# Kernel optimization log

Hardware: AMD Instinct MI355X
Metric: run time of the kernel (lower is better)

Reference implementation:

```python
import jax, jax.numpy as jnp
import numpy as np

D_MODEL = 1024
N_HEADS = 16
D_HEAD = D_MODEL // N_HEADS


def setup_inputs() -> dict:
    key = jax.random.key(0)
    ks = jax.random.split(key, 9)
    B, S = 2, 2048
    s = 0.02
    return {
        "x": jax.random.normal(ks[0], (B, S, D_MODEL), dtype=jnp.float32),
        "Wq": jax.random.normal(ks[1], (D_MODEL, D_MODEL), dtype=jnp.float32) * s,
        "bq": jnp.zeros((D_MODEL,), dtype=jnp.float32),
        "Wk": jax.random.normal(ks[2], (D_MODEL, D_MODEL), dtype=jnp.float32) * s,
        "bk": jnp.zeros((D_MODEL,), dtype=jnp.float32),
        "Wv": jax.random.normal(ks[3], (D_MODEL, D_MODEL), dtype=jnp.float32) * s,
        "bv": jnp.zeros((D_MODEL,), dtype=jnp.float32),
        "Wo": jax.random.normal(ks[4], (D_MODEL, D_MODEL), dtype=jnp.float32) * s,
        "bo": jnp.zeros((D_MODEL,), dtype=jnp.float32),
    }


def reference(x, Wq, bq, Wk, bk, Wv, bv, Wo, bo):
    B, S, _ = x.shape
    # projections -> [B, H, S, Dh]
    def split_heads(t):
        return t.reshape(B, S, N_HEADS, D_HEAD).transpose(0, 2, 1, 3)
    Q = split_heads(x @ Wq + bq)
    K = split_heads(x @ Wk + bk)
    V = split_heads(x @ Wv + bv)
    scores = jnp.einsum('bhqd,bhkd->bhqk', Q, K)  # [B,H,S,S]
    mask = jnp.tril(jnp.ones((S, S), dtype=bool))
    # NB: original masks BEFORE scaling (mask fill -1e9 then /sqrt(d_head))
    scores = jnp.where(mask[None, None], scores, jnp.float32(-1e9))
    scores = scores / jnp.sqrt(jnp.float32(D_HEAD))
    attn = jax.nn.softmax(scores, axis=-1)
    ctx = jnp.einsum('bhqk,bhkd->bhqd', attn, V)
    ctx = ctx.transpose(0, 2, 1, 3).reshape(B, S, D_MODEL)
    return ctx @ Wo + bo
```

## Files before the change

kernel.cpp:

```cpp
#include <hip/hip_runtime.h>

typedef __bf16 bf16;
typedef __bf16 bf16x8 __attribute__((ext_vector_type(8)));
typedef __bf16 bf16x4 __attribute__((ext_vector_type(4)));
typedef float  f32x4  __attribute__((ext_vector_type(4)));

#define D_MODEL 1024
#define S_LEN   2048
#define NHEAD   16
#define DHEAD   64
#define BATCH   2
#define MROWS   (BATCH * S_LEN)

#define QSCALE 0.18033688011112042f

__device__ __forceinline__ void gld_lds16(const void* g, void* lds_base) {
    __builtin_amdgcn_global_load_lds(
        (const __attribute__((address_space(1))) void*)g,
        (__attribute__((address_space(3))) void*)lds_base, 16, 0, 0);
}

__global__ void prep_kernel(const float* __restrict__ x,
                            const float* __restrict__ W0, const float* __restrict__ W1,
                            const float* __restrict__ W2, const float* __restrict__ W3,
                            bf16* __restrict__ xb, bf16* __restrict__ Wt) {
    int tx = threadIdx.x, ty = threadIdx.y;
    if (blockIdx.z == 4) {
        int tid = ty * 32 + tx;
        size_t base = ((size_t)blockIdx.y * 32 + blockIdx.x) * 4096;
#pragma unroll
        for (int j = 0; j < 4; j++) {
            size_t i = base + (size_t)(j * 256 + tid) * 4;
            f32x4 v = *(const f32x4*)(x + i);
            bf16x4 o;
            o[0] = (bf16)v[0]; o[1] = (bf16)v[1]; o[2] = (bf16)v[2]; o[3] = (bf16)v[3];
            *(bf16x4*)(xb + i) = o;
        }
        return;
    }
    __shared__ float tile[32][33];
    const float* W = (blockIdx.z == 0) ? W0 : (blockIdx.z == 1) ? W1
                   : (blockIdx.z == 2) ? W2 : W3;
    int n0 = blockIdx.x * 32, k0 = blockIdx.y * 32;
#pragma unroll
    for (int j = 0; j < 4; j++)
        tile[ty + 8 * j][tx] = W[(size_t)(k0 + ty + 8 * j) * D_MODEL + n0 + tx];
    __syncthreads();
    bf16* out = Wt + (size_t)blockIdx.z * D_MODEL * D_MODEL;
#pragma unroll
    for (int j = 0; j < 4; j++)
        out[(size_t)(n0 + ty + 8 * j) * D_MODEL + k0 + tx] = (bf16)tile[tx][ty + 8 * j];
}

template <int MODE>
__global__ __launch_bounds__(256, 2) void gemm_kernel(
    const bf16* __restrict__ A, const bf16* __restrict__ Bt,
    const float* __restrict__ b0, const float* __restrict__ b1, const float* __restrict__ b2,
    bf16* __restrict__ Qo, bf16* __restrict__ Ko, bf16* __restrict__ Vto,
    float* __restrict__ Co) {
    __shared__ bf16 sA[128 * 32];
    __shared__ bf16 sB[128 * 32];
    const int t = threadIdx.x;
    const int wave = t >> 6, lane = t & 63;
    const int wm = wave >> 1, wn = wave & 1;
    const int quad = lane >> 4, m16 = lane & 15;
    const int row0 = blockIdx.y * 128, col0 = blockIdx.x * 128;
    const int K = D_MODEL;

    f32x4 acc[4][4];
#pragma unroll
    for (int i = 0; i < 4; i++)
#pragma unroll
        for (int j = 0; j < 4; j++) acc[i][j] = (f32x4){0.f, 0.f, 0.f, 0.f};

    for (int kk = 0; kk < K; kk += 32) {
#pragma unroll
        for (int i = 0; i < 2; i++) {
            int cb = i * 256 + wave * 64;
            int c  = cb + lane;
            int r  = c >> 2, kg = c & 3;
            gld_lds16(A  + (size_t)(row0 + r) * K + kk + kg * 8, (char*)sA + cb * 16);
            gld_lds16(Bt + (size_t)(col0 + r) * K + kk + kg * 8, (char*)sB + cb * 16);
        }
        __syncthreads();
        bf16x8 af[4], bfr[4];
#pragma unroll
        for (int mi = 0; mi < 4; mi++)
            af[mi] = *(const bf16x8*)&sA[(wm * 64 + mi * 16 + m16) * 32 + quad * 8];
#pragma unroll
        for (int ni = 0; ni < 4; ni++)
            bfr[ni] = *(const bf16x8*)&sB[(wn * 64 + ni * 16 + m16) * 32 + quad * 8];
#pragma unroll
        for (int mi = 0; mi < 4; mi++)
#pragma unroll
            for (int ni = 0; ni < 4; ni++)
                acc[mi][ni] = __builtin_amdgcn_mfma_f32_16x16x32_bf16(
                    af[mi], bfr[ni], acc[mi][ni], 0, 0, 0);
        __syncthreads();
    }

    if (MODE == 1) {
#pragma unroll
        for (int mi = 0; mi < 4; mi++) {
            int r0 = row0 + wm * 64 + mi * 16 + quad * 4;
#pragma unroll
            for (int ni = 0; ni < 4; ni++) {
                int col = col0 + wn * 64 + ni * 16 + m16;
                float bias = b0[col];
#pragma unroll
                for (int r = 0; r < 4; r++)
                    Co[(size_t)(r0 + r) * D_MODEL + col] = acc[mi][ni][r] + bias;
            }
        }
    } else {
        int sel = col0 >> 10;
        const float* bias_arr = (sel == 0) ? b0 : (sel == 1) ? b1 : b2;
#pragma unroll
        for (int mi = 0; mi < 4; mi++) {
            int s0g = row0 + wm * 64 + mi * 16 + quad * 4;
            int b = s0g >> 11, ss0 = s0g & 2047;
#pragma unroll
            for (int ni = 0; ni < 4; ni++) {
                int col = col0 + wn * 64 + ni * 16 + m16;
                int cn = col & 1023;
                int h = cn >> 6, d = cn & 63;
                float bias = bias_arr[cn];
                if (sel < 2) {
                    bf16* dst = (sel == 0) ? Qo : Ko;
                    float scl = (sel == 0) ? QSCALE : 1.0f;
                    size_t base = (((size_t)b * NHEAD + h) * S_LEN);
#pragma unroll
                    for (int r = 0; r < 4; r++)
                        dst[(base + ss0 + r) * DHEAD + d] = (bf16)((acc[mi][ni][r] + bias) * scl);
                } else {
                    bf16x4 pk;
#pragma unroll
                    for (int r = 0; r < 4; r++) pk[r] = (bf16)(acc[mi][ni][r] + bias);
                    *(bf16x4*)(Vto + (((size_t)b * NHEAD + h) * DHEAD + d) * S_LEN + ss0) = pk;
                }
            }
        }
    }
}

__global__ __launch_bounds__(256, 2) void attn_kernel(
    const bf16* __restrict__ Q, const bf16* __restrict__ K,
    const bf16* __restrict__ Vt, bf16* __restrict__ ctx) {
    __shared__ bf16 Kt_s[3][64 * 64];
    __shared__ bf16 Vt_s[3][64 * 64];
    __shared__ bf16 P_s[4][2][16 * 72];

    const int t = threadIdx.x, wave = t >> 6, lane = t & 63;
    const int quad = lane >> 4, m16 = lane & 15;
    const int bh = blockIdx.y, p = blockIdx.x;
    const int tT[2] = {p, 31 - p};
    const int nt = 32 - p;
    const size_t base = (size_t)bh * S_LEN * DHEAD;

    bf16x8 aq[2][2];
#pragma unroll
    for (int it = 0; it < 2; it++)
#pragma unroll
        for (int kst = 0; kst < 2; kst++)
            aq[it][kst] = *(const bf16x8*)(Q + base
                + (size_t)(tT[it] * 64 + wave * 16 + m16) * DHEAD + kst * 32 + quad * 8);

    f32x4 o[2][4];
#pragma unroll
    for (int it = 0; it < 2; it++)
#pragma unroll
        for (int di = 0; di < 4; di++) o[it][di] = (f32x4){0.f, 0.f, 0.f, 0.f};
    float l_acc[2] = {0.f, 0.f};

    auto stage = [&](int j, int buf) {
#pragma unroll
        for (int i = 0; i < 2; i++) {
            int cb = i * 256 + wave * 64;
            int c  = cb + lane;
            int pos = c >> 3, g = c & 7;
            int gk = g ^ (pos & 7);
            gld_lds16(K  + base + (size_t)(j * 64 + pos) * DHEAD + gk * 8,
                      (char*)&Kt_s[buf][0] + cb * 16);
            gld_lds16(Vt + base + (size_t)pos * S_LEN + j * 64 + gk * 8,
                      (char*)&Vt_s[buf][0] + cb * 16);
        }
    };

    stage(0, 0);
    if (nt > 1) stage(1, 1);

    for (int j = 0; j < nt; ++j) {
        if (j + 1 < nt) asm volatile("s_waitcnt vmcnt(4)\n\ts_barrier" ::: "memory");
        else            asm volatile("s_waitcnt vmcnt(0)\n\ts_barrier" ::: "memory");
        if (j + 2 < nt) stage(j + 2, (j + 2) % 3);

        const int cur = j % 3;
        const bool aAct = (j <= tT[0]);
        const int kt0 = j * 64;

        auto computeTile = [&](bool both) {
            int itlo = both ? 0 : 1;
            f32x4 sc[2][4];
#pragma unroll
            for (int it = 0; it < 2; it++)
#pragma unroll
                for (int ni = 0; ni < 4; ni++) sc[it][ni] = (f32x4){0.f, 0.f, 0.f, 0.f};
#pragma unroll
            for (int ni = 0; ni < 4; ni++) {
                int pos = ni * 16 + m16;
#pragma unroll
                for (int kst = 0; kst < 2; kst++) {
                    int gg = (kst * 4 + quad) ^ (pos & 7);
                    bf16x8 kf = *(const bf16x8*)&Kt_s[cur][pos * 64 + gg * 8];
                    sc[1][ni] = __builtin_amdgcn_mfma_f32_16x16x32_bf16(
                        kf, aq[1][kst], sc[1][ni], 0, 0, 0);
                    if (both)
                        sc[0][ni] = __builtin_amdgcn_mfma_f32_16x16x32_bf16(
                            kf, aq[0][kst], sc[0][ni], 0, 0, 0);
                }
            }
#pragma unroll
            for (int it = 0; it < 2; it++) {
                if (it < itlo) continue;
                if (j == tT[it]) {
                    int qg = tT[it] * 64 + wave * 16 + m16;
#pragma unroll
                    for (int ni = 0; ni < 4; ni++)
#pragma unroll
                        for (int r = 0; r < 4; r++) {
                            int kp = kt0 + ni * 16 + quad * 4 + r;
                            if (kp > qg) sc[it][ni][r] = -1e9f;
                        }
                }
            }
#pragma unroll
            for (int it = 0; it < 2; it++) {
                if (it < itlo) continue;
                bf16* Pw = &P_s[wave][it][0];
                float ls = 0.f;
#pragma unroll
                for (int ni = 0; ni < 4; ni++) {
                    bf16x4 pk;
#pragma unroll
                    for (int r = 0; r < 4; r++) {
                        float pe = __builtin_amdgcn_exp2f(sc[it][ni][r]);
                        ls += pe;
                        pk[r] = (bf16)pe;
                    }
                    *(bf16x4*)&Pw[m16 * 72 + ni * 16 + quad * 4] = pk;
                }
                l_acc[it] += ls;
            }
#pragma unroll
            for (int kst = 0; kst < 2; kst++) {
                bf16x8 ap[2];
#pragma unroll
                for (int it = 0; it < 2; it++)
                    if (it >= itlo)
                        ap[it] = *(const bf16x8*)&P_s[wave][it][m16 * 72 + kst * 32 + quad * 8];
#pragma unroll
                for (int di = 0; di < 4; di++) {
                    int d = di * 16 + m16;
                    int gg = (kst * 4 + quad) ^ (d & 7);
                    bf16x8 vf = *(const bf16x8*)&Vt_s[cur][d * 64 + gg * 8];
                    o[1][di] = __builtin_amdgcn_mfma_f32_16x16x32_bf16(
                        vf, ap[1], o[1][di], 0, 0, 0);
                    if (both)
                        o[0][di] = __builtin_amdgcn_mfma_f32_16x16x32_bf16(
                            vf, ap[0], o[0][di], 0, 0, 0);
                }
            }
        };
        if (aAct) computeTile(true);
        else      computeTile(false);
    }

    int b = bh >> 4, h = bh & 15;
#pragma unroll
    for (int it = 0; it < 2; it++) {
        float l = l_acc[it];
        l += __shfl_xor(l, 16);
        l += __shfl_xor(l, 32);
        float rl = 1.0f / l;
        int s = tT[it] * 64 + wave * 16 + m16;
#pragma unroll
        for (int di = 0; di < 4; di++) {
            bf16x4 pk;
#pragma unroll
            for (int r = 0; r < 4; r++) pk[r] = (bf16)(o[it][di][r] * rl);
            *(bf16x4*)(ctx + ((size_t)b * S_LEN + s) * D_MODEL
                       + h * DHEAD + di * 16 + quad * 4) = pk;
        }
    }
}

extern "C" void kernel_launch(void* const* d_in, const int* in_sizes, int n_in,
                              void* d_out, int out_size, void* d_ws, size_t ws_size,
                              hipStream_t stream) {
    const float* x  = (const float*)d_in[0];
    const float* Wq = (const float*)d_in[1];
    const float* bq = (const float*)d_in[2];
    const float* Wk = (const float*)d_in[3];
    const float* bk = (const float*)d_in[4];
    const float* Wv = (const float*)d_in[5];
    const float* bv = (const float*)d_in[6];
    const float* Wo = (const float*)d_in[7];
    const float* bo = (const float*)d_in[8];
    float* out = (float*)d_out;

    char* ws = (char*)d_ws;
    const size_t MB = 1u << 20;
    bf16* xb  = (bf16*)(ws + 0);
    bf16* Wt  = (bf16*)(ws + 8  * MB);
    bf16* Qb  = (bf16*)(ws + 16 * MB);
    bf16* Kb  = (bf16*)(ws + 24 * MB);
    bf16* Vtb = (bf16*)(ws + 32 * MB);
    bf16* ctx = (bf16*)(ws + 0);

    prep_kernel<<<dim3(32, 32, 5), dim3(32, 8), 0, stream>>>(x, Wq, Wk, Wv, Wo, xb, Wt);
    gemm_kernel<0><<<dim3(24, 32), 256, 0, stream>>>(xb, Wt, bq, bk, bv,
                                                     Qb, Kb, Vtb, nullptr);
    attn_kernel<<<dim3(16, 32), 256, 0, stream>>>(Qb, Kb, Vtb, ctx);
    gemm_kernel<1><<<dim3(8, 32), 256, 0, stream>>>(ctx, Wt + 3 * 1024 * 1024,
                                                    bo, nullptr, nullptr,
                                                    nullptr, nullptr, nullptr, out);
}
```

Measured before the change: 191.0 us.

## Triple-buffer GEMM K-loop and shrink attention LDS for higher occupancy

The GEMM kernel gets a three-stage LDS ring with global_load_lds prefetch two tiles ahead. A single s_waitcnt/s_barrier per iteration replaces the two __syncthreads, so loads overlap the MFMA work. The attention kernel drops from triple to double buffering and shares one P scratch buffer per wave between the two query tiles. This cuts LDS so launch bounds can ask for 3 blocks per CU, but it serializes the two tiles' softmax/PV work and exposes more load latency per iteration.

```diff
diff --git a/kernel.cpp b/kernel.cpp
--- a/kernel.cpp
+++ b/kernel.cpp
@@ -58,14 +58,15 @@
     const float* __restrict__ b0, const float* __restrict__ b1, const float* __restrict__ b2,
     bf16* __restrict__ Qo, bf16* __restrict__ Ko, bf16* __restrict__ Vto,
     float* __restrict__ Co) {
-    __shared__ bf16 sA[128 * 32];
-    __shared__ bf16 sB[128 * 32];
+    __shared__ bf16 sA[3][128 * 32];
+    __shared__ bf16 sB[3][128 * 32];
     const int t = threadIdx.x;
     const int wave = t >> 6, lane = t & 63;
     const int wm = wave >> 1, wn = wave & 1;
     const int quad = lane >> 4, m16 = lane & 15;
     const int row0 = blockIdx.y * 128, col0 = blockIdx.x * 128;
     const int K = D_MODEL;
+    const int NT = K / 32;
 
     f32x4 acc[4][4];
 #pragma unroll
@@ -73,30 +74,41 @@
 #pragma unroll
         for (int j = 0; j < 4; j++) acc[i][j] = (f32x4){0.f, 0.f, 0.f, 0.f};
 
-    for (int kk = 0; kk < K; kk += 32) {
+    auto stage = [&](int j, int buf) {
 #pragma unroll
         for (int i = 0; i < 2; i++) {
             int cb = i * 256 + wave * 64;
             int c  = cb + lane;
             int r  = c >> 2, kg = c & 3;
-            gld_lds16(A  + (size_t)(row0 + r) * K + kk + kg * 8, (char*)sA + cb * 16);
-            gld_lds16(Bt + (size_t)(col0 + r) * K + kk + kg * 8, (char*)sB + cb * 16);
-        }
-        __syncthreads();
+            gld_lds16(A  + (size_t)(row0 + r) * K + j * 32 + kg * 8,
+                      (char*)&sA[buf][0] + cb * 16);
+            gld_lds16(Bt + (size_t)(col0 + r) * K + j * 32 + kg * 8,
+                      (char*)&sB[buf][0] + cb * 16);
+        }
+    };
+
+    stage(0, 0);
+    stage(1, 1);
+
+    for (int j = 0; j < NT; ++j) {
+        if (j + 1 < NT) asm volatile("s_waitcnt vmcnt(4)\n\ts_barrier" ::: "memory");
+        else            asm volatile("s_waitcnt vmcnt(0)\n\ts_barrier" ::: "memory");
+        if (j + 2 < NT) stage(j + 2, (j + 2) % 3);
+        const int cur = j % 3;
+
         bf16x8 af[4], bfr[4];
 #pragma unroll
         for (int mi = 0; mi < 4; mi++)
-            af[mi] = *(const bf16x8*)&sA[(wm * 64 + mi * 16 + m16) * 32 + quad * 8];
+            af[mi] = *(const bf16x8*)&sA[cur][(wm * 64 + mi * 16 + m16) * 32 + quad * 8];
 #pragma unroll
         for (int ni = 0; ni < 4; ni++)
-            bfr[ni] = *(const bf16x8*)&sB[(wn * 64 + ni * 16 + m16) * 32 + quad * 8];
+            bfr[ni] = *(const bf16x8*)&sB[cur][(wn * 64 + ni * 16 + m16) * 32 + quad * 8];
 #pragma unroll
         for (int mi = 0; mi < 4; mi++)
 #pragma unroll
             for (int ni = 0; ni < 4; ni++)
                 acc[mi][ni] = __builtin_amdgcn_mfma_f32_16x16x32_bf16(
                     af[mi], bfr[ni], acc[mi][ni], 0, 0, 0);
-        __syncthreads();
     }
 
     if (MODE == 1) {
@@ -143,12 +155,12 @@
     }
 }
 
-__global__ __launch_bounds__(256, 2) void attn_kernel(
+__global__ __launch_bounds__(256, 3) void attn_kernel(
     const bf16* __restrict__ Q, const bf16* __restrict__ K,
     const bf16* __restrict__ Vt, bf16* __restrict__ ctx) {
-    __shared__ bf16 Kt_s[3][64 * 64];
-    __shared__ bf16 Vt_s[3][64 * 64];
-    __shared__ bf16 P_s[4][2][16 * 72];
+    __shared__ bf16 Kt_s[2][64 * 64];
+    __shared__ bf16 Vt_s[2][64 * 64];
+    __shared__ bf16 P_s[4][16 * 72];
 
     const int t = threadIdx.x, wave = t >> 6, lane = t & 63;
     const int quad = lane >> 4, m16 = lane & 15;
@@ -187,92 +199,74 @@
     };
 
     stage(0, 0);
-    if (nt > 1) stage(1, 1);
 
     for (int j = 0; j < nt; ++j) {
-        if (j + 1 < nt) asm volatile("s_waitcnt vmcnt(4)\n\ts_barrier" ::: "memory");
-        else            asm volatile("s_waitcnt vmcnt(0)\n\ts_barrier" ::: "memory");
-        if (j + 2 < nt) stage(j + 2, (j + 2) % 3);
-
-        const int cur = j % 3;
+        asm volatile("s_waitcnt vmcnt(0)\n\ts_barrier" ::: "memory");
+        if (j + 1 < nt) stage(j + 1, (j + 1) & 1);
+        const int cur = j & 1;
         const bool aAct = (j <= tT[0]);
         const int kt0 = j * 64;
 
-        auto computeTile = [&](bool both) {
-            int itlo = both ? 0 : 1;
-            f32x4 sc[2][4];
-#pragma unroll
-            for (int it = 0; it < 2; it++)
-#pragma unroll
-                for (int ni = 0; ni < 4; ni++) sc[it][ni] = (f32x4){0.f, 0.f, 0.f, 0.f};
+        f32x4 sc[2][4];
+#pragma unroll
+        for (int it = 0; it < 2; it++)
+#pragma unroll
+            for (int ni = 0; ni < 4; ni++) sc[it][ni] = (f32x4){0.f, 0.f, 0.f, 0.f};
+#pragma unroll
+        for (int ni = 0; ni < 4; ni++) {
+            int pos = ni * 16 + m16;
+#pragma unroll
+            for (int kst = 0; kst < 2; kst++) {
+                int gg = (kst * 4 + quad) ^ (pos & 7);
+                bf16x8 kf = *(const bf16x8*)&Kt_s[cur][pos * 64 + gg * 8];
+                sc[1][ni] = __builtin_amdgcn_mfma_f32_16x16x32_bf16(
+                    kf, aq[1][kst], sc[1][ni], 0, 0, 0);
+                if (aAct)
+                    sc[0][ni] = __builtin_amdgcn_mfma_f32_16x16x32_bf16(
+                        kf, aq[0][kst], sc[0][ni], 0, 0, 0);
+            }
+        }
+
+        bf16* Pw = &P_s[wave][0];
+#pragma unroll
+        for (int it = 1; it >= 0; it--) {
+            if (it == 0 && !aAct) continue;
+            if (j == tT[it]) {
+                int qg = tT[it] * 64 + wave * 16 + m16;
+#pragma unroll
+                for (int ni = 0; ni < 4; ni++)
+#pragma unroll
+                    for (int r = 0; r < 4; r++) {
+                        int kp = kt0 + ni * 16 + quad * 4 + r;
+                        if (kp > qg) sc[it][ni][r] = -1e9f;
+                    }
+            }
+            float ls = 0.f;
 #pragma unroll
             for (int ni = 0; ni < 4; ni++) {
-                int pos = ni * 16 + m16;
-#pragma unroll
-                for (int kst = 0; kst < 2; kst++) {
-                    int gg = (kst * 4 + quad) ^ (pos & 7);
-                    bf16x8 kf = *(const bf16x8*)&Kt_s[cur][pos * 64 + gg * 8];
-                    sc[1][ni] = __builtin_amdgcn_mfma_f32_16x16x32_bf16(
-                        kf, aq[1][kst], sc[1][ni], 0, 0, 0);
-                    if (both)
-                        sc[0][ni] = __builtin_amdgcn_mfma_f32_16x16x32_bf16(
-                            kf, aq[0][kst], sc[0][ni], 0, 0, 0);
+                bf16x4 pk;
+#pragma unroll
+                for (int r = 0; r < 4; r++) {
+                    float pe = __builtin_amdgcn_exp2f(sc[it][ni][r]);
+                    ls += pe;
+                    pk[r] = (bf16)pe;
                 }
-            }
-#pragma unroll
-            for (int it = 0; it < 2; it++) {
-                if (it < itlo) continue;
-                if (j == tT[it]) {
-                    int qg = tT[it] * 64 + wave * 16 + m16;
-#pragma unroll
-                    for (int ni = 0; ni < 4; ni++)
-#pragma unroll
-                        for (int r = 0; r < 4; r++) {
-                            int kp = kt0 + ni * 16 + quad * 4 + r;
-                            if (kp > qg) sc[it][ni][r] = -1e9f;
-                        }
-                }
-            }
-#pragma unroll
-            for (int it = 0; it < 2; it++) {
-                if (it < itlo) continue;
-                bf16* Pw = &P_s[wave][it][0];
-                float ls = 0.f;
-#pragma unroll
-                for (int ni = 0; ni < 4; ni++) {
-                    bf16x4 pk;
-#pragma unroll
-                    for (int r = 0; r < 4; r++) {
-                        float pe = __builtin_amdgcn_exp2f(sc[it][ni][r]);
-                        ls += pe;
-                        pk[r] = (bf16)pe;
-                    }
-                    *(bf16x4*)&Pw[m16 * 72 + ni * 16 + quad * 4] = pk;
-                }
-                l_acc[it] += ls;
-            }
+                *(bf16x4*)&Pw[m16 * 72 + ni * 16 + quad * 4] = pk;
+            }
+            l_acc[it] += ls;
 #pragma unroll
             for (int kst = 0; kst < 2; kst++) {
-                bf16x8 ap[2];
-#pragma unroll
-                for (int it = 0; it < 2; it++)
-                    if (it >= itlo)
-                        ap[it] = *(const bf16x8*)&P_s[wave][it][m16 * 72 + kst * 32 + quad * 8];
+                bf16x8 ap = *(const bf16x8*)&Pw[m16 * 72 + kst * 32 + quad * 8];
 #pragma unroll
                 for (int di = 0; di < 4; di++) {
                     int d = di * 16 + m16;
                     int gg = (kst * 4 + quad) ^ (d & 7);
                     bf16x8 vf = *(const bf16x8*)&Vt_s[cur][d * 64 + gg * 8];
-                    o[1][di] = __builtin_amdgcn_mfma_f32_16x16x32_bf16(
-                        vf, ap[1], o[1][di], 0, 0, 0);
-                    if (both)
-                        o[0][di] = __builtin_amdgcn_mfma_f32_16x16x32_bf16(
-                            vf, ap[0], o[0][di], 0, 0, 0);
+                    o[it][di] = __builtin_amdgcn_mfma_f32_16x16x32_bf16(
+                        vf, ap, o[it][di], 0, 0, 0);
                 }
             }
-        };
-        if (aAct) computeTile(true);
-        else      computeTile(false);
+        }
     }
 
     int b = bh >> 4, h = bh & 15;
```

Result: no change. 191.8 us (+0.4%).

## Triple-buffer GEMM LDS loads and vectorize prep kernel stores

Applied to the files above, without the earlier changes.

The GEMM main loop now uses three LDS buffers with asynchronous global-to-LDS prefetch two tiles ahead. Each iteration waits on partial vmcnt plus a single barrier, replacing the load, sync, compute, sync sequence so that memory latency overlaps MFMA work. Occupancy hint raised to 3 blocks per CU. The prep kernel also uses wider bf16 stores (8-wide for x, 4-wide for transposed W) to cut store instruction count. The extra LDS (48KB per block) may limit achievable occupancy, and the hand-written waitcnt relies on the exact count of outstanding loads per stage.

```diff
diff --git a/kernel.cpp b/kernel.cpp
--- a/kernel.cpp
+++ b/kernel.cpp
@@ -27,15 +27,19 @@
     int tx = threadIdx.x, ty = threadIdx.y;
     if (blockIdx.z == 4) {
         int tid = ty * 32 + tx;
-        size_t base = ((size_t)blockIdx.y * 32 + blockIdx.x) * 4096;
-#pragma unroll
-        for (int j = 0; j < 4; j++) {
-            size_t i = base + (size_t)(j * 256 + tid) * 4;
-            f32x4 v = *(const f32x4*)(x + i);
-            bf16x4 o;
-            o[0] = (bf16)v[0]; o[1] = (bf16)v[1]; o[2] = (bf16)v[2]; o[3] = (bf16)v[3];
-            *(bf16x4*)(xb + i) = o;
-        }
+        size_t base = ((size_t)blockIdx.y * 32 + blockIdx.x) * 4096 + (size_t)tid * 16;
+        f32x4 v0 = *(const f32x4*)(x + base);
+        f32x4 v1 = *(const f32x4*)(x + base + 4);
+        f32x4 v2 = *(const f32x4*)(x + base + 8);
+        f32x4 v3 = *(const f32x4*)(x + base + 12);
+        bf16x8 o0, o1;
+#pragma unroll
+        for (int r = 0; r < 4; r++) {
+            o0[r] = (bf16)v0[r]; o0[r + 4] = (bf16)v1[r];
+            o1[r] = (bf16)v2[r]; o1[r + 4] = (bf16)v3[r];
+        }
+        *(bf16x8*)(xb + base)     = o0;
+        *(bf16x8*)(xb + base + 8) = o1;
         return;
     }
     __shared__ float tile[32][33];
@@ -47,25 +51,29 @@
         tile[ty + 8 * j][tx] = W[(size_t)(k0 + ty + 8 * j) * D_MODEL + n0 + tx];
     __syncthreads();
     bf16* out = Wt + (size_t)blockIdx.z * D_MODEL * D_MODEL;
-#pragma unroll
-    for (int j = 0; j < 4; j++)
-        out[(size_t)(n0 + ty + 8 * j) * D_MODEL + k0 + tx] = (bf16)tile[tx][ty + 8 * j];
+    int nn = ty + 8 * (tx >> 3);
+    int k4 = (tx & 7) * 4;
+    bf16x4 pk;
+#pragma unroll
+    for (int r = 0; r < 4; r++) pk[r] = (bf16)tile[k4 + r][nn];
+    *(bf16x4*)(out + (size_t)(n0 + nn) * D_MODEL + k0 + k4) = pk;
 }
 
 template <int MODE>
-__global__ __launch_bounds__(256, 2) void gemm_kernel(
+__global__ __launch_bounds__(256, 3) void gemm_kernel(
     const bf16* __restrict__ A, const bf16* __restrict__ Bt,
     const float* __restrict__ b0, const float* __restrict__ b1, const float* __restrict__ b2,
     bf16* __restrict__ Qo, bf16* __restrict__ Ko, bf16* __restrict__ Vto,
     float* __restrict__ Co) {
-    __shared__ bf16 sA[128 * 32];
-    __shared__ bf16 sB[128 * 32];
+    __shared__ bf16 sA[3][128 * 32];
+    __shared__ bf16 sB[3][128 * 32];
     const int t = threadIdx.x;
     const int wave = t >> 6, lane = t & 63;
     const int wm = wave >> 1, wn = wave & 1;
     const int quad = lane >> 4, m16 = lane & 15;
     const int row0 = blockIdx.y * 128, col0 = blockIdx.x * 128;
     const int K = D_MODEL;
+    const int NT = K / 32;
 
     f32x4 acc[4][4];
 #pragma unroll
@@ -73,30 +81,41 @@
 #pragma unroll
         for (int j = 0; j < 4; j++) acc[i][j] = (f32x4){0.f, 0.f, 0.f, 0.f};
 
-    for (int kk = 0; kk < K; kk += 32) {
+    auto stage = [&](int j, int buf) {
 #pragma unroll
         for (int i = 0; i < 2; i++) {
             int cb = i * 256 + wave * 64;
             int c  = cb + lane;
             int r  = c >> 2, kg = c & 3;
-            gld_lds16(A  + (size_t)(row0 + r) * K + kk + kg * 8, (char*)sA + cb * 16);
-            gld_lds16(Bt + (size_t)(col0 + r) * K + kk + kg * 8, (char*)sB + cb * 16);
-        }
-        __syncthreads();
+            gld_lds16(A  + (size_t)(row0 + r) * K + j * 32 + kg * 8,
+                      (char*)&sA[buf][0] + cb * 16);
+            gld_lds16(Bt + (size_t)(col0 + r) * K + j * 32 + kg * 8,
+                      (char*)&sB[buf][0] + cb * 16);
+        }
+    };
+
+    stage(0, 0);
+    stage(1, 1);
+
+    for (int j = 0; j < NT; ++j) {
+        if (j + 1 < NT) asm volatile("s_waitcnt vmcnt(4)\n\ts_barrier" ::: "memory");
+        else            asm volatile("s_waitcnt vmcnt(0)\n\ts_barrier" ::: "memory");
+        if (j + 2 < NT) stage(j + 2, (j + 2) % 3);
+        const int cur = j % 3;
+
         bf16x8 af[4], bfr[4];
 #pragma unroll
         for (int mi = 0; mi < 4; mi++)
-            af[mi] = *(const bf16x8*)&sA[(wm * 64 + mi * 16 + m16) * 32 + quad * 8];
+            af[mi] = *(const bf16x8*)&sA[cur][(wm * 64 + mi * 16 + m16) * 32 + quad * 8];
 #pragma unroll
         for (int ni = 0; ni < 4; ni++)
-            bfr[ni] = *(const bf16x8*)&sB[(wn * 64 + ni * 16 + m16) * 32 + quad * 8];
+            bfr[ni] = *(const bf16x8*)&sB[cur][(wn * 64 + ni * 16 + m16) * 32 + quad * 8];
 #pragma unroll
         for (int mi = 0; mi < 4; mi++)
 #pragma unroll
             for (int ni = 0; ni < 4; ni++)
                 acc[mi][ni] = __builtin_amdgcn_mfma_f32_16x16x32_bf16(
                     af[mi], bfr[ni], acc[mi][ni], 0, 0, 0);
-        __syncthreads();
     }
 
     if (MODE == 1) {
```

After: 194.1 us. Within noise of the previous version (+1.6%).
